# Optimization experiments

Hardware: AMD Instinct MI355X
Metric: run time of the kernel (lower is better)

The kernel has to match this reference:

```python
import jax, jax.numpy as jnp
import numpy as np

N = 100000
E = 3200000
IN = 128
HID = 128   # 2 * out_channels
OUT = 64


def setup_inputs() -> dict:
    key = jax.random.key(0)
    ks = jax.random.split(key, 8)
    x = jax.random.normal(ks[0], (N, IN), dtype=jnp.float32)
    edge_index = jax.random.randint(ks[1], (2, E), 0, N, dtype=jnp.int64)
    s1 = 1.0 / np.sqrt(IN)
    s2 = 1.0 / np.sqrt(HID)
    # PyG GraphConv per layer: lin_rel (with bias) applied to aggregated neighbors,
    # lin_root (no bias) applied to the node itself. Linear weight is (out, in).
    W1_rel = jax.random.uniform(ks[2], (HID, IN), jnp.float32, -s1, s1)
    b1 = jax.random.uniform(ks[3], (HID,), jnp.float32, -s1, s1)
    W1_root = jax.random.uniform(ks[4], (HID, IN), jnp.float32, -s1, s1)
    W2_rel = jax.random.uniform(ks[5], (OUT, HID), jnp.float32, -s2, s2)
    b2 = jax.random.uniform(ks[6], (OUT,), jnp.float32, -s2, s2)
    W2_root = jax.random.uniform(ks[7], (OUT, HID), jnp.float32, -s2, s2)
    return {"x": x, "edge_index": edge_index, "W1_rel": W1_rel, "b1": b1,
            "W1_root": W1_root, "W2_rel": W2_rel, "b2": b2, "W2_root": W2_root}


def _graph_conv(h, src, dst, W_rel, b, W_root, num_nodes):
    # sum-aggregate neighbor features at dst, then affine combine with root term
    agg = jax.ops.segment_sum(h[src], dst, num_segments=num_nodes)  # [N, d_in]
    return agg @ W_rel.T + b + h @ W_root.T


def reference(x, edge_index, W1_rel, b1, W1_root, W2_rel, b2, W2_root):
    src = edge_index[0]
    dst = edge_index[1]
    n = x.shape[0]
    h = _graph_conv(x, src, dst, W1_rel, b1, W1_root, n)
    h = jax.nn.relu(h)  # dropout p=0.0 -> identity
    return _graph_conv(h, src, dst, W2_rel, b2, W2_root, n)
```

## Files before the change

kernel.cpp:

```cpp
#include <hip/hip_runtime.h>
#include <hip/hip_bf16.h>


#define EB 8192
#define NB_MAX 512

typedef __attribute__((ext_vector_type(8))) short bf16x8;
typedef __attribute__((ext_vector_type(4))) float f32x4;
typedef __attribute__((ext_vector_type(2))) float f32x2;

__device__ __forceinline__ uint pack_bf16x2(float a, float b) {
    __hip_bfloat162 p = __float22bfloat162_rn(make_float2(a, b));
    return *(uint*)&p;
}

__device__ __forceinline__ uchar pack_fp8(float v) {
    uint p = __builtin_amdgcn_cvt_pk_fp8_f32(v, v, 0, false);
    return (uchar)(p & 0xff);
}

__device__ __forceinline__ float bflo(uint g) { return __uint_as_float(g << 16); }
__device__ __forceinline__ float bfhi(uint g) { return __uint_as_float(g & 0xffff0000u); }


__global__ __launch_bounds__(256) void bucket_hist(const int* __restrict__ dst, int E,
                                                   int NB, int* __restrict__ hist) {
    __shared__ int h[NB_MAX];
    int t = threadIdx.x;
    for (int i = t; i < NB; i += 256) h[i] = 0;
    __syncthreads();
    int e0 = blockIdx.x * EB, e1 = min(E, e0 + EB);
    for (int e = e0 + t; e < e1; e += 256) atomicAdd(&h[dst[e] >> 8], 1);
    __syncthreads();
    int* row = hist + (size_t)blockIdx.x * NB;
    for (int i = t; i < NB; i += 256) row[i] = h[i];
}

__global__ __launch_bounds__(256) void scan_blocks(int* __restrict__ hist, int NBLK,
                                                   int NB, int* __restrict__ total) {
    __shared__ int s[256];
    __shared__ int carry;
    int b = blockIdx.x, t = threadIdx.x;
    if (t == 0) carry = 0;
    __syncthreads();
    for (int start = 0; start < NBLK; start += 256) {
        int i = start + t;
        int v = (i < NBLK) ? hist[(size_t)i * NB + b] : 0;
        s[t] = v;
        __syncthreads();
        for (int off = 1; off < 256; off <<= 1) {
            int u = (t >= off) ? s[t - off] : 0;
            __syncthreads();
            s[t] += u;
            __syncthreads();
        }
        if (i < NBLK) hist[(size_t)i * NB + b] = carry + s[t] - v;
        __syncthreads();
        if (t == 255) carry += s[255];
        __syncthreads();
    }
    if (t == 0) total[b] = carry;
}

__global__ __launch_bounds__(512) void scan_total(const int* __restrict__ total, int NB,
                                                  int* __restrict__ base) {
    __shared__ int s[512];
    int t = threadIdx.x;
    int v = (t < NB) ? total[t] : 0;
    s[t] = v;
    __syncthreads();
    for (int off = 1; off < 512; off <<= 1) {
        int u = (t >= off) ? s[t - off] : 0;
        __syncthreads();
        s[t] += u;
        __syncthreads();
    }
    if (t < NB) base[t] = s[t] - v;
}

__global__ __launch_bounds__(256) void bucket_scatter(const int* __restrict__ src,
                                                      const int* __restrict__ dst, int E,
                                                      int NB, const int* __restrict__ hist,
                                                      const int* __restrict__ base,
                                                      uint* __restrict__ ebuf) {
    __shared__ int cur[NB_MAX];
    int t = threadIdx.x, blk = blockIdx.x;
    const int* row = hist + (size_t)blk * NB;
    for (int i = t; i < NB; i += 256) cur[i] = base[i] + row[i];
    __syncthreads();
    int e0 = blk * EB, e1 = min(E, e0 + EB);
    for (int e = e0 + t; e < e1; e += 256) {
        int d = dst[e];
        int p = atomicAdd(&cur[d >> 8], 1);
        ebuf[p] = ((uint)(d & 255) << 24) | (uint)src[e];
    }
}

__global__ __launch_bounds__(256) void build_csr_bucket(const uint* __restrict__ ebuf,
                                                        const int* __restrict__ base,
                                                        const int* __restrict__ total,
                                                        int NB, int N, int E,
                                                        int* __restrict__ rowptr,
                                                        int* __restrict__ col) {
    __shared__ int cnt[256];
    __shared__ int s[256];
    __shared__ int cur[256];
    int b = blockIdx.x, t = threadIdx.x;
    int e0 = base[b], e1 = e0 + total[b];
    cnt[t] = 0;
    __syncthreads();
    for (int e = e0 + t; e < e1; e += 256) atomicAdd(&cnt[ebuf[e] >> 24], 1);
    __syncthreads();
    int v = cnt[t];
    s[t] = v;
    __syncthreads();
    for (int off = 1; off < 256; off <<= 1) {
        int u = (t >= off) ? s[t - off] : 0;
        __syncthreads();
        s[t] += u;
        __syncthreads();
    }
    int start = e0 + s[t] - v;
    int node = (b << 8) + t;
    if (node < N) rowptr[node] = start;
    if (b == NB - 1 && t == 0) rowptr[N] = E;
    cur[t] = start;
    __syncthreads();
    for (int e = e0 + t; e < e1; e += 256) {
        uint ev = ebuf[e];
        int p = atomicAdd(&cur[ev >> 24], 1);
        col[p] = (int)(ev & 0xFFFFFFu);
    }
}


#define LDK 72

template <int C, bool A_BF16, bool Y_FP8>
__global__ __launch_bounds__(256, 2) void gemm_mfma(const void* __restrict__ Aptr,
                                                    const float* __restrict__ Wa,
                                                    const float* __restrict__ Wb,
                                                    const float* __restrict__ bias,
                                                    void* __restrict__ Yout,
                                                    float* __restrict__ Z, int n_rows) {
    __shared__ ushort Xs[128 * LDK];
    __shared__ ushort Ws[128 * LDK];

    const int t = threadIdx.x;
    const int lane = t & 63;
    const int wave = t >> 6;
    const int wm = wave >> 1, wn = wave & 1;
    const int row0 = blockIdx.x * 128;
    const int tn = blockIdx.y;
    const int fr = lane & 15;
    const int quad = lane >> 4;

    f32x4 acc[4][4];
#pragma unroll
    for (int i = 0; i < 4; i++)
#pragma unroll
        for (int j = 0; j < 4; j++) acc[i][j] = (f32x4){0.f, 0.f, 0.f, 0.f};

    for (int ko = 0; ko < 2; ++ko) {
        if (A_BF16) {
            const ushort* A = (const ushort*)Aptr;
#pragma unroll
            for (int j = 0; j < 4; ++j) {
                int f = j * 256 + t;
                int r = f >> 3, c = f & 7;
                int grow = row0 + r;
                uint4 v = make_uint4(0u, 0u, 0u, 0u);
                if (grow < n_rows)
                    v = *(const uint4*)(A + (size_t)grow * 128 + ko * 64 + c * 8);
                *(uint4*)(&Xs[r * LDK + c * 8]) = v;
            }
        } else {
            const float* A = (const float*)Aptr;
#pragma unroll
            for (int j = 0; j < 8; ++j) {
                int f = j * 256 + t;
                int r = f >> 4, c = f & 15;
                int grow = row0 + r;
                float4 v = make_float4(0.f, 0.f, 0.f, 0.f);
                if (grow < n_rows)
                    v = *(const float4*)(A + (size_t)grow * 128 + ko * 64 + c * 4);
                uint2 u;
                u.x = pack_bf16x2(v.x, v.y);
                u.y = pack_bf16x2(v.z, v.w);
                *(uint2*)(&Xs[r * LDK + c * 4]) = u;
            }
        }
#pragma unroll
        for (int j = 0; j < 8; ++j) {
            int f = j * 256 + t;
            int r = f >> 4, c = f & 15;
            int grow = tn * 128 + r;
            const float* Wr = (grow < C) ? (Wa + (size_t)grow * 128)
                                         : (Wb + (size_t)(grow - C) * 128);
            float4 v = *(const float4*)(Wr + ko * 64 + c * 4);
            uint2 u;
            u.x = pack_bf16x2(v.x, v.y);
            u.y = pack_bf16x2(v.z, v.w);
            *(uint2*)(&Ws[r * LDK + c * 4]) = u;
        }
        __syncthreads();

#pragma unroll
        for (int ks = 0; ks < 2; ++ks) {
            bf16x8 a[4], b[4];
#pragma unroll
            for (int mt = 0; mt < 4; ++mt)
                a[mt] = *(const bf16x8*)(&Xs[(wm * 64 + mt * 16 + fr) * LDK +
                                             ks * 32 + quad * 8]);
#pragma unroll
            for (int nt = 0; nt < 4; ++nt)
                b[nt] = *(const bf16x8*)(&Ws[(wn * 64 + nt * 16 + fr) * LDK +
                                             ks * 32 + quad * 8]);
#pragma unroll
            for (int mt = 0; mt < 4; ++mt)
#pragma unroll
                for (int nt = 0; nt < 4; ++nt)
                    acc[mt][nt] = __builtin_amdgcn_mfma_f32_16x16x32_bf16(
                        a[mt], b[nt], acc[mt][nt], 0, 0, 0);
        }
        __syncthreads();
    }

#pragma unroll
    for (int nt = 0; nt < 4; ++nt) {
        int gcol = tn * 128 + wn * 64 + nt * 16 + fr;
        if (gcol < C) {
#pragma unroll
            for (int mt = 0; mt < 4; ++mt) {
#pragma unroll
                for (int r = 0; r < 4; ++r) {
                    int grow = row0 + wm * 64 + mt * 16 + quad * 4 + r;
                    if (grow < n_rows) {
                        if (Y_FP8) {
                            ((uchar*)Yout)[(size_t)grow * C + gcol] =
                                pack_fp8(acc[mt][nt][r]);
                        } else {
                            __hip_bfloat16 hb = __float2bfloat16(acc[mt][nt][r]);
                            ((ushort*)Yout)[(size_t)grow * C + gcol] = *(ushort*)&hb;
                        }
                    }
                }
            }
        } else {
            float bv = bias[gcol - C];
#pragma unroll
            for (int mt = 0; mt < 4; ++mt) {
#pragma unroll
                for (int r = 0; r < 4; ++r) {
                    int grow = row0 + wm * 64 + mt * 16 + quad * 4 + r;
                    if (grow < n_rows)
                        Z[(size_t)grow * C + (gcol - C)] = acc[mt][nt][r] + bv;
                }
            }
        }
    }
}


__global__ __launch_bounds__(256) void agg_relu_l1(const uchar* __restrict__ Y1,
                                                   const float* __restrict__ Z1,
                                                   const int* __restrict__ rowptr,
                                                   const int* __restrict__ col,
                                                   ushort* __restrict__ h, int n_nodes) {
    int node = (blockIdx.x * 256 + threadIdx.x) >> 6;
    if (node >= n_nodes) return;
    int lane = threadIdx.x & 63;
    int sub = lane >> 3;
    int cg  = lane & 7;
    int beg = rowptr[node], end = rowptr[node + 1];
    float acc[16];
#pragma unroll
    for (int i = 0; i < 16; i++) acc[i] = 0.f;

    int e = beg;
    for (; e + 16 <= end; e += 16) {
        int s0 = col[e + sub];
        int s1 = col[e + 8 + sub];
        uint4 v0 = *(const uint4*)(Y1 + (size_t)s0 * 128 + cg * 16);
        uint4 v1 = *(const uint4*)(Y1 + (size_t)s1 * 128 + cg * 16);
        f32x2 p;
        p = __builtin_amdgcn_cvt_pk_f32_fp8(v0.x, false); acc[0] += p[0]; acc[1] += p[1];
        p = __builtin_amdgcn_cvt_pk_f32_fp8(v0.x, true);  acc[2] += p[0]; acc[3] += p[1];
        p = __builtin_amdgcn_cvt_pk_f32_fp8(v0.y, false); acc[4] += p[0]; acc[5] += p[1];
        p = __builtin_amdgcn_cvt_pk_f32_fp8(v0.y, true);  acc[6] += p[0]; acc[7] += p[1];
        p = __builtin_amdgcn_cvt_pk_f32_fp8(v0.z, false); acc[8] += p[0]; acc[9] += p[1];
        p = __builtin_amdgcn_cvt_pk_f32_fp8(v0.z, true);  acc[10] += p[0]; acc[11] += p[1];
        p = __builtin_amdgcn_cvt_pk_f32_fp8(v0.w, false); acc[12] += p[0]; acc[13] += p[1];
        p = __builtin_amdgcn_cvt_pk_f32_fp8(v0.w, true);  acc[14] += p[0]; acc[15] += p[1];
        p = __builtin_amdgcn_cvt_pk_f32_fp8(v1.x, false); acc[0] += p[0]; acc[1] += p[1];
        p = __builtin_amdgcn_cvt_pk_f32_fp8(v1.x, true);  acc[2] += p[0]; acc[3] += p[1];
        p = __builtin_amdgcn_cvt_pk_f32_fp8(v1.y, false); acc[4] += p[0]; acc[5] += p[1];
        p = __builtin_amdgcn_cvt_pk_f32_fp8(v1.y, true);  acc[6] += p[0]; acc[7] += p[1];
        p = __builtin_amdgcn_cvt_pk_f32_fp8(v1.z, false); acc[8] += p[0]; acc[9] += p[1];
        p = __builtin_amdgcn_cvt_pk_f32_fp8(v1.z, true);  acc[10] += p[0]; acc[11] += p[1];
        p = __builtin_amdgcn_cvt_pk_f32_fp8(v1.w, false); acc[12] += p[0]; acc[13] += p[1];
        p = __builtin_amdgcn_cvt_pk_f32_fp8(v1.w, true);  acc[14] += p[0]; acc[15] += p[1];
    }
    for (; e < end; e += 8) {
        int ee = e + sub;
        uint4 v = make_uint4(0u, 0u, 0u, 0u);
        if (ee < end)
            v = *(const uint4*)(Y1 + (size_t)col[ee] * 128 + cg * 16);
        f32x2 p;
        p = __builtin_amdgcn_cvt_pk_f32_fp8(v.x, false); acc[0] += p[0]; acc[1] += p[1];
        p = __builtin_amdgcn_cvt_pk_f32_fp8(v.x, true);  acc[2] += p[0]; acc[3] += p[1];
        p = __builtin_amdgcn_cvt_pk_f32_fp8(v.y, false); acc[4] += p[0]; acc[5] += p[1];
        p = __builtin_amdgcn_cvt_pk_f32_fp8(v.y, true);  acc[6] += p[0]; acc[7] += p[1];
        p = __builtin_amdgcn_cvt_pk_f32_fp8(v.z, false); acc[8] += p[0]; acc[9] += p[1];
        p = __builtin_amdgcn_cvt_pk_f32_fp8(v.z, true);  acc[10] += p[0]; acc[11] += p[1];
        p = __builtin_amdgcn_cvt_pk_f32_fp8(v.w, false); acc[12] += p[0]; acc[13] += p[1];
        p = __builtin_amdgcn_cvt_pk_f32_fp8(v.w, true);  acc[14] += p[0]; acc[15] += p[1];
    }

#pragma unroll
    for (int off = 8; off < 64; off <<= 1)
#pragma unroll
        for (int i = 0; i < 16; i++) acc[i] += __shfl_xor(acc[i], off, 64);

    if (sub == 0) {
        const float4* zp = (const float4*)(Z1 + (size_t)node * 128 + cg * 16);
        uint o[8];
#pragma unroll
        for (int q = 0; q < 4; ++q) {
            float4 z = zp[q];
            float r0 = acc[q * 4 + 0] + z.x;
            float r1 = acc[q * 4 + 1] + z.y;
            float r2 = acc[q * 4 + 2] + z.z;
            float r3 = acc[q * 4 + 3] + z.w;
            r0 = r0 > 0.f ? r0 : 0.f;
            r1 = r1 > 0.f ? r1 : 0.f;
            r2 = r2 > 0.f ? r2 : 0.f;
            r3 = r3 > 0.f ? r3 : 0.f;
            o[q * 2 + 0] = pack_bf16x2(r0, r1);
            o[q * 2 + 1] = pack_bf16x2(r2, r3);
        }
        uint* hp = (uint*)(h + (size_t)node * 128) + cg * 8;
        *(uint4*)(hp + 0) = make_uint4(o[0], o[1], o[2], o[3]);
        *(uint4*)(hp + 4) = make_uint4(o[4], o[5], o[6], o[7]);
    }
}


__global__ __launch_bounds__(256) void agg_l2(const ushort* __restrict__ Y2,
                                              const float* __restrict__ Z2,
                                              const int* __restrict__ rowptr,
                                              const int* __restrict__ col,
                                              float* __restrict__ out, int n_nodes) {
    int node = (blockIdx.x * 256 + threadIdx.x) >> 6;
    if (node >= n_nodes) return;
    int lane = threadIdx.x & 63;
    int sub = lane >> 3;
    int cg  = lane & 7;
    int beg = rowptr[node], end = rowptr[node + 1];
    float acc[8];
#pragma unroll
    for (int i = 0; i < 8; i++) acc[i] = 0.f;

    int e = beg;
    for (; e + 16 <= end; e += 16) {
        int s0 = col[e + sub];
        int s1 = col[e + 8 + sub];
        uint4 v0 = *(const uint4*)(Y2 + (size_t)s0 * 64 + cg * 8);
        uint4 v1 = *(const uint4*)(Y2 + (size_t)s1 * 64 + cg * 8);
        acc[0] += bflo(v0.x) + bflo(v1.x);
        acc[1] += bfhi(v0.x) + bfhi(v1.x);
        acc[2] += bflo(v0.y) + bflo(v1.y);
        acc[3] += bfhi(v0.y) + bfhi(v1.y);
        acc[4] += bflo(v0.z) + bflo(v1.z);
        acc[5] += bfhi(v0.z) + bfhi(v1.z);
        acc[6] += bflo(v0.w) + bflo(v1.w);
        acc[7] += bfhi(v0.w) + bfhi(v1.w);
    }
    for (; e < end; e += 8) {
        int ee = e + sub;
        uint4 v = make_uint4(0u, 0u, 0u, 0u);
        if (ee < end)
            v = *(const uint4*)(Y2 + (size_t)col[ee] * 64 + cg * 8);
        acc[0] += bflo(v.x);
        acc[1] += bfhi(v.x);
        acc[2] += bflo(v.y);
        acc[3] += bfhi(v.y);
        acc[4] += bflo(v.z);
        acc[5] += bfhi(v.z);
        acc[6] += bflo(v.w);
        acc[7] += bfhi(v.w);
    }

#pragma unroll
    for (int off = 8; off < 64; off <<= 1)
#pragma unroll
        for (int i = 0; i < 8; i++) acc[i] += __shfl_xor(acc[i], off, 64);

    if (sub == 0) {
        const float4* zp = (const float4*)(Z2 + (size_t)node * 64 + cg * 8);
        float4 z0 = zp[0], z1 = zp[1];
        float4 o0 = {acc[0] + z0.x, acc[1] + z0.y, acc[2] + z0.z, acc[3] + z0.w};
        float4 o1 = {acc[4] + z1.x, acc[5] + z1.y, acc[6] + z1.z, acc[7] + z1.w};
        float4* op = (float4*)(out + (size_t)node * 64 + cg * 8);
        op[0] = o0;
        op[1] = o1;
    }
}


extern "C" void kernel_launch(void* const* d_in, const int* in_sizes, int n_in,
                              void* d_out, int out_size, void* d_ws, size_t ws_size,
                              hipStream_t stream) {
    const float* x       = (const float*)d_in[0];
    const int*   ei      = (const int*)d_in[1];
    const float* W1_rel  = (const float*)d_in[2];
    const float* b1      = (const float*)d_in[3];
    const float* W1_root = (const float*)d_in[4];
    const float* W2_rel  = (const float*)d_in[5];
    const float* b2      = (const float*)d_in[6];
    const float* W2_root = (const float*)d_in[7];
    float* out = (float*)d_out;

    const int N = in_sizes[0] / 128;
    const int E = in_sizes[1] / 2;
    const int* srcA = ei;
    const int* dstA = ei + E;
    const int NB   = (N + 255) >> 8;
    const int NBLK = (E + EB - 1) / EB;

    char* ws = (char*)d_ws;
    size_t cur = 0;
    auto alloc = [&](size_t bytes) -> void* {
        size_t o = cur;
        cur = (cur + bytes + 511) & ~(size_t)511;
        return (void*)(ws + o);
    };
    uchar*  Y1  = (uchar*)alloc((size_t)N * 128);
    float*  Z1  = (float*)alloc((size_t)N * 128 * 4);
    ushort* h   = (ushort*)alloc((size_t)N * 128 * 2);
    ushort* Y2  = (ushort*)alloc((size_t)N * 64 * 2);
    float*  Z2  = (float*)alloc((size_t)N * 64 * 4);
    int* rowptr = (int*)alloc((size_t)(N + 1) * 4);
    int* colA   = (int*)alloc((size_t)E * 4);
    int* hist   = (int*)alloc((size_t)NBLK * NB * 4);
    int* btotal = (int*)alloc((size_t)NB_MAX * 4);
    int* bbase  = (int*)alloc((size_t)NB_MAX * 4);
    uint* ebuf  = (uint*)h;

    bucket_hist<<<NBLK, 256, 0, stream>>>(dstA, E, NB, hist);
    scan_blocks<<<NB, 256, 0, stream>>>(hist, NBLK, NB, btotal);
    scan_total<<<1, 512, 0, stream>>>(btotal, NB, bbase);
    bucket_scatter<<<NBLK, 256, 0, stream>>>(srcA, dstA, E, NB, hist, bbase, ebuf);
    build_csr_bucket<<<NB, 256, 0, stream>>>(ebuf, bbase, btotal, NB, N, E, rowptr, colA);

    const int gblk = (N + 127) / 128;
    gemm_mfma<128, false, true><<<dim3(gblk, 2), 256, 0, stream>>>(
        x, W1_rel, W1_root, b1, Y1, Z1, N);
    agg_relu_l1<<<(N + 3) / 4, 256, 0, stream>>>(Y1, Z1, rowptr, colA, h, N);
    gemm_mfma<64, true, false><<<dim3(gblk, 1), 256, 0, stream>>>(
        h, W2_rel, W2_root, b2, Y2, Z2, N);
    agg_l2<<<(N + 3) / 4, 256, 0, stream>>>(Y2, Z2, rowptr, colA, out, N);
}
```

Measured before the change: 425.2 us.

## Pre-convert weights to bf16, read B from global, widen aggregation unroll

Adds a prep kernel that converts both layers' weights to bf16 once. The GEMM now loads the full K=128 A tile into shared memory in a single pass and reads weight fragments straight from global/L2, which removes the weight LDS staging, one sync round, and per-block fp32->bf16 weight conversion. Occupancy hint goes from 2 to 4 blocks. Both aggregation kernels unroll to 32 edges per iteration for more loads in flight, at the cost of more registers and a longer tail loop.

```diff
diff --git a/kernel.cpp b/kernel.cpp
--- a/kernel.cpp
+++ b/kernel.cpp
@@ -17,6 +17,11 @@
 __device__ __forceinline__ uchar pack_fp8(float v) {
     uint p = __builtin_amdgcn_cvt_pk_fp8_f32(v, v, 0, false);
     return (uchar)(p & 0xff);
+}
+
+__device__ __forceinline__ ushort f2bf(float v) {
+    __hip_bfloat16 b = __float2bfloat16(v);
+    return *(ushort*)&b;
 }
 
 __device__ __forceinline__ float bflo(uint g) { return __uint_as_float(g << 16); }
@@ -134,17 +139,32 @@
 }
 
 
-#define LDK 72
+__global__ __launch_bounds__(256) void prep_w(const float* __restrict__ W1_rel,
+                                              const float* __restrict__ W1_root,
+                                              const float* __restrict__ W2_rel,
+                                              const float* __restrict__ W2_root,
+                                              ushort* __restrict__ Wb1,
+                                              ushort* __restrict__ Wb2) {
+    int i = blockIdx.x * 256 + threadIdx.x;
+    if (i < 32768)
+        Wb1[i] = f2bf((i < 16384) ? W1_rel[i] : W1_root[i - 16384]);
+    else {
+        int j = i - 32768;
+        if (j < 16384)
+            Wb2[j] = f2bf((j < 8192) ? W2_rel[j] : W2_root[j - 8192]);
+    }
+}
+
+
+#define LDK2 136
 
 template <int C, bool A_BF16, bool Y_FP8>
-__global__ __launch_bounds__(256, 2) void gemm_mfma(const void* __restrict__ Aptr,
-                                                    const float* __restrict__ Wa,
-                                                    const float* __restrict__ Wb,
+__global__ __launch_bounds__(256, 4) void gemm_mfma(const void* __restrict__ Aptr,
+                                                    const ushort* __restrict__ Wst,
                                                     const float* __restrict__ bias,
                                                     void* __restrict__ Yout,
                                                     float* __restrict__ Z, int n_rows) {
-    __shared__ ushort Xs[128 * LDK];
-    __shared__ ushort Ws[128 * LDK];
+    __shared__ ushort Xs[128 * LDK2];
 
     const int t = threadIdx.x;
     const int lane = t & 63;
@@ -155,75 +175,58 @@
     const int fr = lane & 15;
     const int quad = lane >> 4;
 
-    f32x4 acc[4][4];
-#pragma unroll
-    for (int i = 0; i < 4; i++)
-#pragma unroll
-        for (int j = 0; j < 4; j++) acc[i][j] = (f32x4){0.f, 0.f, 0.f, 0.f};
-
-    for (int ko = 0; ko < 2; ++ko) {
-        if (A_BF16) {
-            const ushort* A = (const ushort*)Aptr;
-#pragma unroll
-            for (int j = 0; j < 4; ++j) {
-                int f = j * 256 + t;
-                int r = f >> 3, c = f & 7;
-                int grow = row0 + r;
-                uint4 v = make_uint4(0u, 0u, 0u, 0u);
-                if (grow < n_rows)
-                    v = *(const uint4*)(A + (size_t)grow * 128 + ko * 64 + c * 8);
-                *(uint4*)(&Xs[r * LDK + c * 8]) = v;
-            }
-        } else {
-            const float* A = (const float*)Aptr;
-#pragma unroll
-            for (int j = 0; j < 8; ++j) {
-                int f = j * 256 + t;
-                int r = f >> 4, c = f & 15;
-                int grow = row0 + r;
-                float4 v = make_float4(0.f, 0.f, 0.f, 0.f);
-                if (grow < n_rows)
-                    v = *(const float4*)(A + (size_t)grow * 128 + ko * 64 + c * 4);
-                uint2 u;
-                u.x = pack_bf16x2(v.x, v.y);
-                u.y = pack_bf16x2(v.z, v.w);
-                *(uint2*)(&Xs[r * LDK + c * 4]) = u;
-            }
-        }
+    if (A_BF16) {
+        const ushort* A = (const ushort*)Aptr;
 #pragma unroll
         for (int j = 0; j < 8; ++j) {
             int f = j * 256 + t;
             int r = f >> 4, c = f & 15;
-            int grow = tn * 128 + r;
-            const float* Wr = (grow < C) ? (Wa + (size_t)grow * 128)
-                                         : (Wb + (size_t)(grow - C) * 128);
-            float4 v = *(const float4*)(Wr + ko * 64 + c * 4);
+            int grow = row0 + r;
+            uint4 v = make_uint4(0u, 0u, 0u, 0u);
+            if (grow < n_rows) v = *(const uint4*)(A + (size_t)grow * 128 + c * 8);
+            *(uint4*)(&Xs[r * LDK2 + c * 8]) = v;
+        }
+    } else {
+        const float* A = (const float*)Aptr;
+#pragma unroll
+        for (int j = 0; j < 16; ++j) {
+            int f = j * 256 + t;
+            int r = f >> 5, c = f & 31;
+            int grow = row0 + r;
+            float4 v = make_float4(0.f, 0.f, 0.f, 0.f);
+            if (grow < n_rows) v = *(const float4*)(A + (size_t)grow * 128 + c * 4);
             uint2 u;
             u.x = pack_bf16x2(v.x, v.y);
             u.y = pack_bf16x2(v.z, v.w);
-            *(uint2*)(&Ws[r * LDK + c * 4]) = u;
+            *(uint2*)(&Xs[r * LDK2 + c * 4]) = u;
         }
-        __syncthreads();
-
-#pragma unroll
-        for (int ks = 0; ks < 2; ++ks) {
-            bf16x8 a[4], b[4];
-#pragma unroll
-            for (int mt = 0; mt < 4; ++mt)
-                a[mt] = *(const bf16x8*)(&Xs[(wm * 64 + mt * 16 + fr) * LDK +
-                                             ks * 32 + quad * 8]);
+    }
+    __syncthreads();
+
+    f32x4 acc[4][4];
+#pragma unroll
+    for (int i = 0; i < 4; i++)
+#pragma unroll
+        for (int j = 0; j < 4; j++) acc[i][j] = (f32x4){0.f, 0.f, 0.f, 0.f};
+
+#pragma unroll
+    for (int ks = 0; ks < 4; ++ks) {
+        bf16x8 a[4], b[4];
+#pragma unroll
+        for (int nt = 0; nt < 4; ++nt)
+            b[nt] = *(const bf16x8*)(Wst +
+                     (size_t)(tn * 128 + wn * 64 + nt * 16 + fr) * 128 +
+                     ks * 32 + quad * 8);
+#pragma unroll
+        for (int mt = 0; mt < 4; ++mt)
+            a[mt] = *(const bf16x8*)(&Xs[(wm * 64 + mt * 16 + fr) * LDK2 +
+                                         ks * 32 + quad * 8]);
+#pragma unroll
+        for (int mt = 0; mt < 4; ++mt)
 #pragma unroll
             for (int nt = 0; nt < 4; ++nt)
-                b[nt] = *(const bf16x8*)(&Ws[(wn * 64 + nt * 16 + fr) * LDK +
-                                             ks * 32 + quad * 8]);
-#pragma unroll
-            for (int mt = 0; mt < 4; ++mt)
-#pragma unroll
-                for (int nt = 0; nt < 4; ++nt)
-                    acc[mt][nt] = __builtin_amdgcn_mfma_f32_16x16x32_bf16(
-                        a[mt], b[nt], acc[mt][nt], 0, 0, 0);
-        }
-        __syncthreads();
+                acc[mt][nt] = __builtin_amdgcn_mfma_f32_16x16x32_bf16(
+                    a[mt], b[nt], acc[mt][nt], 0, 0, 0);
     }
 
 #pragma unroll
@@ -236,13 +239,12 @@
                 for (int r = 0; r < 4; ++r) {
                     int grow = row0 + wm * 64 + mt * 16 + quad * 4 + r;
                     if (grow < n_rows) {
-                        if (Y_FP8) {
+                        if (Y_FP8)
                             ((uchar*)Yout)[(size_t)grow * C + gcol] =
                                 pack_fp8(acc[mt][nt][r]);
-                        } else {
-                            __hip_bfloat16 hb = __float2bfloat16(acc[mt][nt][r]);
-                            ((ushort*)Yout)[(size_t)grow * C + gcol] = *(ushort*)&hb;
-                        }
+                        else
+                            ((ushort*)Yout)[(size_t)grow * C + gcol] =
+                                f2bf(acc[mt][nt][r]);
                     }
                 }
             }
@@ -261,6 +263,17 @@
     }
 }
 
+
+__device__ __forceinline__ void acc_fp8x16(f32x2* acc2, uint4 v) {
+    acc2[0] += __builtin_amdgcn_cvt_pk_f32_fp8(v.x, false);
+    acc2[1] += __builtin_amdgcn_cvt_pk_f32_fp8(v.x, true);
+    acc2[2] += __builtin_amdgcn_cvt_pk_f32_fp8(v.y, false);
+    acc2[3] += __builtin_amdgcn_cvt_pk_f32_fp8(v.y, true);
+    acc2[4] += __builtin_amdgcn_cvt_pk_f32_fp8(v.z, false);
+    acc2[5] += __builtin_amdgcn_cvt_pk_f32_fp8(v.z, true);
+    acc2[6] += __builtin_amdgcn_cvt_pk_f32_fp8(v.w, false);
+    acc2[7] += __builtin_amdgcn_cvt_pk_f32_fp8(v.w, true);
+}
 
 __global__ __launch_bounds__(256) void agg_relu_l1(const uchar* __restrict__ Y1,
                                                    const float* __restrict__ Z1,
@@ -273,50 +286,35 @@
     int sub = lane >> 3;
     int cg  = lane & 7;
     int beg = rowptr[node], end = rowptr[node + 1];
-    float acc[16];
-#pragma unroll
-    for (int i = 0; i < 16; i++) acc[i] = 0.f;
+    f32x2 acc2[8];
+#pragma unroll
+    for (int i = 0; i < 8; i++) acc2[i] = (f32x2){0.f, 0.f};
 
     int e = beg;
-    for (; e + 16 <= end; e += 16) {
+    for (; e + 32 <= end; e += 32) {
         int s0 = col[e + sub];
         int s1 = col[e + 8 + sub];
+        int s2 = col[e + 16 + sub];
+        int s3 = col[e + 24 + sub];
         uint4 v0 = *(const uint4*)(Y1 + (size_t)s0 * 128 + cg * 16);
         uint4 v1 = *(const uint4*)(Y1 + (size_t)s1 * 128 + cg * 16);
-        f32x2 p;
-        p = __builtin_amdgcn_cvt_pk_f32_fp8(v0.x, false); acc[0] += p[0]; acc[1] += p[1];
-        p = __builtin_amdgcn_cvt_pk_f32_fp8(v0.x, true);  acc[2] += p[0]; acc[3] += p[1];
-        p = __builtin_amdgcn_cvt_pk_f32_fp8(v0.y, false); acc[4] += p[0]; acc[5] += p[1];
-        p = __builtin_amdgcn_cvt_pk_f32_fp8(v0.y, true);  acc[6] += p[0]; acc[7] += p[1];
-        p = __builtin_amdgcn_cvt_pk_f32_fp8(v0.z, false); acc[8] += p[0]; acc[9] += p[1];
-        p = __builtin_amdgcn_cvt_pk_f32_fp8(v0.z, true);  acc[10] += p[0]; acc[11] += p[1];
-        p = __builtin_amdgcn_cvt_pk_f32_fp8(v0.w, false); acc[12] += p[0]; acc[13] += p[1];
-        p = __builtin_amdgcn_cvt_pk_f32_fp8(v0.w, true);  acc[14] += p[0]; acc[15] += p[1];
-        p = __builtin_amdgcn_cvt_pk_f32_fp8(v1.x, false); acc[0] += p[0]; acc[1] += p[1];
-        p = __builtin_amdgcn_cvt_pk_f32_fp8(v1.x, true);  acc[2] += p[0]; acc[3] += p[1];
-        p = __builtin_amdgcn_cvt_pk_f32_fp8(v1.y, false); acc[4] += p[0]; acc[5] += p[1];
-        p = __builtin_amdgcn_cvt_pk_f32_fp8(v1.y, true);  acc[6] += p[0]; acc[7] += p[1];
-        p = __builtin_amdgcn_cvt_pk_f32_fp8(v1.z, false); acc[8] += p[0]; acc[9] += p[1];
-        p = __builtin_amdgcn_cvt_pk_f32_fp8(v1.z, true);  acc[10] += p[0]; acc[11] += p[1];
-        p = __builtin_amdgcn_cvt_pk_f32_fp8(v1.w, false); acc[12] += p[0]; acc[13] += p[1];
-        p = __builtin_amdgcn_cvt_pk_f32_fp8(v1.w, true);  acc[14] += p[0]; acc[15] += p[1];
+        uint4 v2 = *(const uint4*)(Y1 + (size_t)s2 * 128 + cg * 16);
+        uint4 v3 = *(const uint4*)(Y1 + (size_t)s3 * 128 + cg * 16);
+        acc_fp8x16(acc2, v0);
+        acc_fp8x16(acc2, v1);
+        acc_fp8x16(acc2, v2);
+        acc_fp8x16(acc2, v3);
     }
     for (; e < end; e += 8) {
         int ee = e + sub;
         uint4 v = make_uint4(0u, 0u, 0u, 0u);
-        if (ee < end)
-            v = *(const uint4*)(Y1 + (size_t)col[ee] * 128 + cg * 16);
-        f32x2 p;
-        p = __builtin_amdgcn_cvt_pk_f32_fp8(v.x, false); acc[0] += p[0]; acc[1] += p[1];
-        p = __builtin_amdgcn_cvt_pk_f32_fp8(v.x, true);  acc[2] += p[0]; acc[3] += p[1];
-        p = __builtin_amdgcn_cvt_pk_f32_fp8(v.y, false); acc[4] += p[0]; acc[5] += p[1];
-        p = __builtin_amdgcn_cvt_pk_f32_fp8(v.y, true);  acc[6] += p[0]; acc[7] += p[1];
-        p = __builtin_amdgcn_cvt_pk_f32_fp8(v.z, false); acc[8] += p[0]; acc[9] += p[1];
-        p = __builtin_amdgcn_cvt_pk_f32_fp8(v.z, true);  acc[10] += p[0]; acc[11] += p[1];
-        p = __builtin_amdgcn_cvt_pk_f32_fp8(v.w, false); acc[12] += p[0]; acc[13] += p[1];
-        p = __builtin_amdgcn_cvt_pk_f32_fp8(v.w, true);  acc[14] += p[0]; acc[15] += p[1];
-    }
-
+        if (ee < end) v = *(const uint4*)(Y1 + (size_t)col[ee] * 128 + cg * 16);
+        acc_fp8x16(acc2, v);
+    }
+
+    float acc[16];
+#pragma unroll
+    for (int i = 0; i < 8; i++) { acc[2 * i] = acc2[i][0]; acc[2 * i + 1] = acc2[i][1]; }
 #pragma unroll
     for (int off = 8; off < 64; off <<= 1)
 #pragma unroll
@@ -346,6 +344,17 @@
 }
 
 
+__device__ __forceinline__ void acc_bf16x8(float* acc, uint4 v) {
+    acc[0] += bflo(v.x);
+    acc[1] += bfhi(v.x);
+    acc[2] += bflo(v.y);
+    acc[3] += bfhi(v.y);
+    acc[4] += bflo(v.z);
+    acc[5] += bfhi(v.z);
+    acc[6] += bflo(v.w);
+    acc[7] += bfhi(v.w);
+}
+
 __global__ __launch_bounds__(256) void agg_l2(const ushort* __restrict__ Y2,
                                               const float* __restrict__ Z2,
                                               const int* __restrict__ rowptr,
@@ -362,33 +371,25 @@
     for (int i = 0; i < 8; i++) acc[i] = 0.f;
 
     int e = beg;
-    for (; e + 16 <= end; e += 16) {
+    for (; e + 32 <= end; e += 32) {
         int s0 = col[e + sub];
         int s1 = col[e + 8 + sub];
+        int s2 = col[e + 16 + sub];
+        int s3 = col[e + 24 + sub];
         uint4 v0 = *(const uint4*)(Y2 + (size_t)s0 * 64 + cg * 8);
         uint4 v1 = *(const uint4*)(Y2 + (size_t)s1 * 64 + cg * 8);
-        acc[0] += bflo(v0.x) + bflo(v1.x);
-        acc[1] += bfhi(v0.x) + bfhi(v1.x);
-        acc[2] += bflo(v0.y) + bflo(v1.y);
-        acc[3] += bfhi(v0.y) + bfhi(v1.y);
-        acc[4] += bflo(v0.z) + bflo(v1.z);
-        acc[5] += bfhi(v0.z) + bfhi(v1.z);
-        acc[6] += bflo(v0.w) + bflo(v1.w);
-        acc[7] += bfhi(v0.w) + bfhi(v1.w);
+        uint4 v2 = *(const uint4*)(Y2 + (size_t)s2 * 64 + cg * 8);
+        uint4 v3 = *(const uint4*)(Y2 + (size_t)s3 * 64 + cg * 8);
+        acc_bf16x8(acc, v0);
+        acc_bf16x8(acc, v1);
+        acc_bf16x8(acc, v2);
+        acc_bf16x8(acc, v3);
     }
     for (; e < end; e += 8) {
         int ee = e + sub;
         uint4 v = make_uint4(0u, 0u, 0u, 0u);
-        if (ee < end)
-            v = *(const uint4*)(Y2 + (size_t)col[ee] * 64 + cg * 8);
-        acc[0] += bflo(v.x);
-        acc[1] += bfhi(v.x);
-        acc[2] += bflo(v.y);
-        acc[3] += bfhi(v.y);
-        acc[4] += bflo(v.z);
-        acc[5] += bfhi(v.z);
-        acc[6] += bflo(v.w);
-        acc[7] += bfhi(v.w);
+        if (ee < end) v = *(const uint4*)(Y2 + (size_t)col[ee] * 64 + cg * 8);
+        acc_bf16x8(acc, v);
     }
 
 #pragma unroll
@@ -440,6 +441,8 @@
     ushort* h   = (ushort*)alloc((size_t)N * 128 * 2);
     ushort* Y2  = (ushort*)alloc((size_t)N * 64 * 2);
     float*  Z2  = (float*)alloc((size_t)N * 64 * 4);
+    ushort* Wb1 = (ushort*)alloc(32768 * 2);
+    ushort* Wb2 = (ushort*)alloc(16384 * 2);
     int* rowptr = (int*)alloc((size_t)(N + 1) * 4);
     int* colA   = (int*)alloc((size_t)E * 4);
     int* hist   = (int*)alloc((size_t)NBLK * NB * 4);
@@ -447,6 +450,7 @@
     int* bbase  = (int*)alloc((size_t)NB_MAX * 4);
     uint* ebuf  = (uint*)h;
 
+    prep_w<<<192, 256, 0, stream>>>(W1_rel, W1_root, W2_rel, W2_root, Wb1, Wb2);
     bucket_hist<<<NBLK, 256, 0, stream>>>(dstA, E, NB, hist);
     scan_blocks<<<NB, 256, 0, stream>>>(hist, NBLK, NB, btotal);
     scan_total<<<1, 512, 0, stream>>>(btotal, NB, bbase);
@@ -455,9 +459,9 @@
 
     const int gblk = (N + 127) / 128;
     gemm_mfma<128, false, true><<<dim3(gblk, 2), 256, 0, stream>>>(
-        x, W1_rel, W1_root, b1, Y1, Z1, N);
+        x, Wb1, b1, Y1, Z1, N);
     agg_relu_l1<<<(N + 3) / 4, 256, 0, stream>>>(Y1, Z1, rowptr, colA, h, N);
     gemm_mfma<64, true, false><<<dim3(gblk, 1), 256, 0, stream>>>(
-        h, W2_rel, W2_root, b2, Y2, Z2, N);
+        h, Wb2, b2, Y2, Z2, N);
     agg_l2<<<(N + 3) / 4, 256, 0, stream>>>(Y2, Z2, rowptr, colA, out, N);
 }
```

Result: slower. 442.9 us (+4.2%).
